# Kernel tuning notes

Measured on AMD Instinct MI355X. Metric: run time of the kernel, lower is better.

The kernel has to match this reference:

```python
import jax, jax.numpy as jnp
import numpy as np


def setup_inputs() -> dict:
    key = jax.random.key(0)
    ks = jax.random.split(key, 8)
    B, C, H, W = 8, 256, 64, 64
    Cqk = C // 8
    x = jax.random.normal(ks[0], (B, C, H, W), dtype=jnp.float32)
    # 1x1 conv weights, stored as [out_ch, in_ch] (kernel is 1x1)
    Wq = jax.random.normal(ks[1], (Cqk, C), dtype=jnp.float32) * 0.02
    bq = jnp.zeros((Cqk,), dtype=jnp.float32)
    Wk = jax.random.normal(ks[2], (Cqk, C), dtype=jnp.float32) * 0.02
    bk = jnp.zeros((Cqk,), dtype=jnp.float32)
    Wv = jax.random.normal(ks[3], (C, C), dtype=jnp.float32) * 0.02
    bv = jnp.zeros((C,), dtype=jnp.float32)
    # gamma initialized to zero in the module; use small nonzero so grads flow through attention path meaningfully
    gamma = jnp.asarray([0.5], dtype=jnp.float32)
    return {"x": x, "Wq": Wq, "bq": bq, "Wk": Wk, "bk": bk, "Wv": Wv, "bv": bv, "gamma": gamma}


def reference(x, Wq, bq, Wk, bk, Wv, bv, gamma):
    B, C, H, W = x.shape
    N = H * W
    xf = x.reshape(B, C, N)  # [B, C, N]
    # 1x1 convs == channel-wise matmuls
    q = jnp.einsum('oc,bcn->bno', Wq, xf) + bq  # [B, N, Cqk]
    k = jnp.einsum('oc,bcn->bon', Wk, xf) + bk[None, :, None]  # [B, Cqk, N]
    v = jnp.einsum('oc,bcn->bon', Wv, xf) + bv[None, :, None]  # [B, C, N]
    energy = jnp.einsum('bnd,bdm->bnm', q, k)  # [B, N, N], unscaled as in original
    attn = jax.nn.softmax(energy, axis=-1)
    out = jnp.einsum('bcm,bnm->bcn', v, attn)  # out[:, :, n] = sum_m v[:, :, m] * attn[n, m]
    out = out.reshape(B, C, H, W)
    return gamma[0] * out + x
```

## Files before the change

### kernel.cpp

```cpp
#include <hip/hip_runtime.h>
#include <hip/hip_bf16.h>

#define NB 8
#define CH 256
#define NN 4096
#define CQK 32
#define LOG2E 1.4426950408889634f

typedef __attribute__((ext_vector_type(4))) float f32x4;
typedef __attribute__((ext_vector_type(8))) short bf16x8;
typedef unsigned short u16;

static __device__ __forceinline__ u16 f2bf(float f) {
  unsigned int u = __float_as_uint(f);
  unsigned int r = (u + 0x7fffu + ((u >> 16) & 1u)) >> 16;
  return (u16)r;
}

__global__ void prep_weights(const float* __restrict__ Wq, const float* __restrict__ bq,
                             const float* __restrict__ Wk, const float* __restrict__ bk,
                             const float* __restrict__ Wv,
                             u16* __restrict__ Wqkf, u16* __restrict__ Wvf,
                             float* __restrict__ bqk) {
  int i = blockIdx.x * 256 + threadIdx.x;
  int o = i >> 8, c = i & 255;
  int kk = c >> 5, g2 = (c >> 3) & 3, j = c & 7;
  if (o < 64) {
    float wv = (o < 32) ? Wq[o * 256 + c] * LOG2E : Wk[(o - 32) * 256 + c];
    Wqkf[((((o >> 4) * 8 + kk) * 4 + g2) * 16 + (o & 15)) * 8 + j] = f2bf(wv);
  }
  Wvf[((((o >> 4) * 8 + kk) * 4 + g2) * 16 + (o & 15)) * 8 + j] = f2bf(Wv[i]);
  if (i < 64) bqk[i] = (i < 32) ? bq[i] * LOG2E : bk[i - 32];
}

__global__ __launch_bounds__(256, 2) void fused_proj(
    const float* __restrict__ x, const u16* __restrict__ Wqkf,
    const u16* __restrict__ Wvf, const float* __restrict__ bqk,
    const float* __restrict__ bv,
    u16* __restrict__ qbuf, u16* __restrict__ kbuf, u16* __restrict__ vbuf) {
  __shared__ __align__(128) char xt[64 * 512];
  const int b = blockIdx.y, n0 = blockIdx.x * 64;
  const int tid = threadIdx.x, w = tid >> 6, l = tid & 63, g = l >> 4, lr = l & 15;
  const f32x4 fzero = {0.f, 0.f, 0.f, 0.f};

  {
    const int nl = l, cl = w;
    const float* xp = x + (size_t)b * CH * NN + n0 + nl;
    char* xrow = xt + nl * 512;
    const int swz = (nl & 15) << 4;
#pragma unroll
    for (int p = 0; p < 32; ++p) {
      const int c = p * 8 + cl * 2;
      float f0 = xp[(size_t)c * NN], f1 = xp[(size_t)(c + 1) * NN];
      unsigned int pk = (unsigned int)f2bf(f0) | ((unsigned int)f2bf(f1) << 16);
      *(unsigned int*)(xrow + ((c * 2) ^ swz)) = pk;
    }
  }
  __syncthreads();

  const int aswz = lr << 4;

  {
    f32x4 acc[4];
#pragma unroll
    for (int ct = 0; ct < 4; ++ct) acc[ct] = fzero;
#pragma unroll
    for (int kk = 0; kk < 8; ++kk) {
      bf16x8 af = *(const bf16x8*)(xt + (w * 16 + lr) * 512 + ((kk * 64 + g * 16) ^ aswz));
#pragma unroll
      for (int ct = 0; ct < 4; ++ct) {
        bf16x8 bf = *(const bf16x8*)(Wqkf + (size_t)(((ct * 8 + kk) * 4 + g) * 16 + lr) * 8);
        acc[ct] = __builtin_amdgcn_mfma_f32_16x16x32_bf16(af, bf, acc[ct], 0, 0, 0);
      }
    }
#pragma unroll
    for (int ct = 0; ct < 4; ++ct) {
      const int col = ct * 16 + lr;
      const float bc = bqk[col];
#pragma unroll
      for (int r = 0; r < 4; ++r) {
        const int row = n0 + w * 16 + g * 4 + r;
        u16 h = f2bf(acc[ct][r] + bc);
        if (col < 32) qbuf[((size_t)(b * NN + row)) * 32 + col] = h;
        else          kbuf[((size_t)(b * NN + row)) * 32 + (col - 32)] = h;
      }
    }
  }

  {
    f32x4 vacc[4][4];
#pragma unroll
    for (int ct = 0; ct < 4; ++ct)
#pragma unroll
      for (int mt = 0; mt < 4; ++mt) vacc[ct][mt] = fzero;
#pragma unroll
    for (int kk = 0; kk < 8; ++kk) {
      bf16x8 bfm[4];
#pragma unroll
      for (int mt = 0; mt < 4; ++mt)
        bfm[mt] = *(const bf16x8*)(xt + (mt * 16 + lr) * 512 + ((kk * 64 + g * 16) ^ aswz));
#pragma unroll
      for (int ct = 0; ct < 4; ++ct) {
        bf16x8 af = *(const bf16x8*)(Wvf + (size_t)((((w * 4 + ct) * 8 + kk) * 4 + g) * 16 + lr) * 8);
#pragma unroll
        for (int mt = 0; mt < 4; ++mt)
          vacc[ct][mt] = __builtin_amdgcn_mfma_f32_16x16x32_bf16(af, bfm[mt], vacc[ct][mt], 0, 0, 0);
      }
    }
#pragma unroll
    for (int ct = 0; ct < 4; ++ct) {
#pragma unroll
      for (int mt = 0; mt < 4; ++mt) {
        const int m = n0 + mt * 16 + lr;
#pragma unroll
        for (int r = 0; r < 4; ++r) {
          const int ch = w * 64 + ct * 16 + g * 4 + r;
          vbuf[((size_t)(b * 128 + (m >> 5)) * 256 + ch) * 32 + (m & 31)] = f2bf(vacc[ct][mt][r] + bv[ch]);
        }
      }
    }
  }
}

#define KLOAD(t, sub) (*(const bf16x8*)(kp + (size_t)((((t) & 63) * 64) + (sub) * 16) * 32))
#define VLOAD(mg, ct) (*(const bf16x8*)(vp + (size_t)((mg) & 127) * 8192 + (ct) * 512))

#define EXPP(S, PW, MASK) {                                                                   \
  float e0 = __builtin_amdgcn_exp2f(S[0]);                                                    \
  float e1 = __builtin_amdgcn_exp2f(S[1]);                                                    \
  float e2 = __builtin_amdgcn_exp2f(S[2]);                                                    \
  float e3 = __builtin_amdgcn_exp2f(S[3]);                                                    \
  lsum += (MASK) * ((e0 + e1) + (e2 + e3));                                                   \
  PW.x = __builtin_amdgcn_perm(__float_as_uint(e1) + 0x8000u, __float_as_uint(e0) + 0x8000u, 0x07060302u); \
  PW.y = __builtin_amdgcn_perm(__float_as_uint(e3) + 0x8000u, __float_as_uint(e2) + 0x8000u, 0x07060302u); \
}

#define PBAR() do {                                  \
  __builtin_amdgcn_sched_barrier(0);                 \
  asm volatile("s_waitcnt lgkmcnt(0)");              \
  __builtin_amdgcn_s_barrier();                      \
  __builtin_amdgcn_sched_barrier(0);                 \
} while (0)

#define PVPH(BUF, NEXTMG) {                                                                   \
  const char* prb = (const char*)Pb + (BUF) * 16384;                                          \
  char* pdst = (char*)Pb + ((BUF) ^ 1) * 16384 + prow * 128;                                  \
  *(uint2*)(pdst + ((0 * 32 + g * 8) ^ wswz)) = pw0;                                          \
  *(uint2*)(pdst + ((1 * 32 + g * 8) ^ wswz)) = pw1;                                          \
  *(uint2*)(pdst + ((2 * 32 + g * 8) ^ wswz)) = pw2;                                          \
  *(uint2*)(pdst + ((3 * 32 + g * 8) ^ wswz)) = pw3;                                          \
  __builtin_amdgcn_s_setprio(1);                                                              \
  _Pragma("unroll")                                                                           \
  for (int nt = 0; nt < 4; ++nt) {                                                            \
    const int row = qg * 64 + nt * 16 + lr;                                                   \
    const int rs = (row & 7) << 4;                                                            \
    bf16x8 pa = *(const bf16x8*)(prb + row * 128 + ((g * 16) ^ rs));                          \
    oacc[nt][0] = __builtin_amdgcn_mfma_f32_16x16x32_bf16(vA0, pa, oacc[nt][0], 0, 0, 0);     \
    oacc[nt][1] = __builtin_amdgcn_mfma_f32_16x16x32_bf16(vA1, pa, oacc[nt][1], 0, 0, 0);     \
    oacc[nt][2] = __builtin_amdgcn_mfma_f32_16x16x32_bf16(vA2, pa, oacc[nt][2], 0, 0, 0);     \
    oacc[nt][3] = __builtin_amdgcn_mfma_f32_16x16x32_bf16(vA3, pa, oacc[nt][3], 0, 0, 0);     \
  }                                                                                           \
  vA0 = VLOAD(NEXTMG, 0); vA1 = VLOAD(NEXTMG, 1);                                             \
  vA2 = VLOAD(NEXTMG, 2); vA3 = VLOAD(NEXTMG, 3);                                             \
  _Pragma("unroll")                                                                           \
  for (int nt = 0; nt < 4; ++nt) {                                                            \
    const int row = qg * 64 + nt * 16 + lr;                                                   \
    const int rs = (row & 7) << 4;                                                            \
    bf16x8 pa = *(const bf16x8*)(prb + row * 128 + ((64 + g * 16) ^ rs));                     \
    oacc[nt][0] = __builtin_amdgcn_mfma_f32_16x16x32_bf16(vB0, pa, oacc[nt][0], 0, 0, 0);     \
    oacc[nt][1] = __builtin_amdgcn_mfma_f32_16x16x32_bf16(vB1, pa, oacc[nt][1], 0, 0, 0);     \
    oacc[nt][2] = __builtin_amdgcn_mfma_f32_16x16x32_bf16(vB2, pa, oacc[nt][2], 0, 0, 0);     \
    oacc[nt][3] = __builtin_amdgcn_mfma_f32_16x16x32_bf16(vB3, pa, oacc[nt][3], 0, 0, 0);     \
  }                                                                                           \
  __builtin_amdgcn_s_setprio(0);                                                              \
}

__global__ __launch_bounds__(512, 2) void attn_fused(
    const u16* __restrict__ qb, const u16* __restrict__ kbuf,
    const u16* __restrict__ vbuf, const float* __restrict__ x,
    const float* __restrict__ gamma_p, float* __restrict__ out) {
  __shared__ __align__(128) char Pb[2][128 * 128];
  __shared__ float lsum_s[128];

  const int b = blockIdx.x;
  const int n0 = blockIdx.y * 128;
  const int tid = threadIdx.x, w = tid >> 6, l = tid & 63, g = l >> 4, lr = l & 15;
  const int qg = w >> 2, cg = w & 3;
  const float gamma0 = gamma_p[0];
  const f32x4 fzero = {0.f, 0.f, 0.f, 0.f};

  bf16x8 qf = *(const bf16x8*)(qb + ((size_t)b * NN + n0 + w * 16 + lr) * 32 + g * 8);

  const u16* kp = kbuf + (size_t)b * (NN * 32) + (size_t)lr * 32 + g * 8;
  const u16* vp = vbuf + (size_t)b * 1048576 + (size_t)(cg * 64 + lr) * 32 + g * 8;

  f32x4 oacc[4][4];
#pragma unroll
  for (int nt = 0; nt < 4; ++nt)
#pragma unroll
    for (int ct = 0; ct < 4; ++ct) oacc[nt][ct] = fzero;
  float lsum = 0.f;

  const int prow = w * 16 + lr;
  const int wswz = (prow & 7) << 4;

  bf16x8 kA0 = KLOAD(0, 0), kA1 = KLOAD(0, 1), kA2 = KLOAD(0, 2), kA3 = KLOAD(0, 3);
  bf16x8 vA0 = VLOAD(0, 0), vA1 = VLOAD(0, 1), vA2 = VLOAD(0, 2), vA3 = VLOAD(0, 3);
  bf16x8 kB0 = KLOAD(1, 0), kB1 = KLOAD(1, 1), kB2 = KLOAD(1, 2), kB3 = KLOAD(1, 3);
  bf16x8 vB0, vB1, vB2, vB3;
  uint2 pw0, pw1, pw2, pw3;
  {
    f32x4 s0 = __builtin_amdgcn_mfma_f32_16x16x32_bf16(kA0, qf, fzero, 0, 0, 0);
    f32x4 s1 = __builtin_amdgcn_mfma_f32_16x16x32_bf16(kA1, qf, fzero, 0, 0, 0);
    f32x4 s2 = __builtin_amdgcn_mfma_f32_16x16x32_bf16(kA2, qf, fzero, 0, 0, 0);
    f32x4 s3 = __builtin_amdgcn_mfma_f32_16x16x32_bf16(kA3, qf, fzero, 0, 0, 0);
    EXPP(s0, pw0, 1.0f); EXPP(s1, pw1, 1.0f); EXPP(s2, pw2, 1.0f); EXPP(s3, pw3, 1.0f);
    char* pdst = (char*)Pb + prow * 128;
    *(uint2*)(pdst + ((0 * 32 + g * 8) ^ wswz)) = pw0;
    *(uint2*)(pdst + ((1 * 32 + g * 8) ^ wswz)) = pw1;
    *(uint2*)(pdst + ((2 * 32 + g * 8) ^ wswz)) = pw2;
    *(uint2*)(pdst + ((3 * 32 + g * 8) ^ wswz)) = pw3;
  }

  for (int it2 = 0; it2 < 32; ++it2) {
    {
      const int tn = 2 * it2 + 1;
      f32x4 s0 = __builtin_amdgcn_mfma_f32_16x16x32_bf16(kB0, qf, fzero, 0, 0, 0);
      f32x4 s1 = __builtin_amdgcn_mfma_f32_16x16x32_bf16(kB1, qf, fzero, 0, 0, 0);
      f32x4 s2 = __builtin_amdgcn_mfma_f32_16x16x32_bf16(kB2, qf, fzero, 0, 0, 0);
      f32x4 s3 = __builtin_amdgcn_mfma_f32_16x16x32_bf16(kB3, qf, fzero, 0, 0, 0);
      kA0 = KLOAD(tn + 1, 0); kA1 = KLOAD(tn + 1, 1); kA2 = KLOAD(tn + 1, 2); kA3 = KLOAD(tn + 1, 3);
      vB0 = VLOAD(4 * it2 + 1, 0); vB1 = VLOAD(4 * it2 + 1, 1);
      vB2 = VLOAD(4 * it2 + 1, 2); vB3 = VLOAD(4 * it2 + 1, 3);
      EXPP(s0, pw0, 1.0f); EXPP(s1, pw1, 1.0f); EXPP(s2, pw2, 1.0f); EXPP(s3, pw3, 1.0f);
      PBAR();
      PVPH(0, 4 * it2 + 2);
    }
    {
      const int tn = 2 * it2 + 2;
      const float tmask = (it2 < 31) ? 1.0f : 0.0f;
      f32x4 s0 = __builtin_amdgcn_mfma_f32_16x16x32_bf16(kA0, qf, fzero, 0, 0, 0);
      f32x4 s1 = __builtin_amdgcn_mfma_f32_16x16x32_bf16(kA1, qf, fzero, 0, 0, 0);
      f32x4 s2 = __builtin_amdgcn_mfma_f32_16x16x32_bf16(kA2, qf, fzero, 0, 0, 0);
      f32x4 s3 = __builtin_amdgcn_mfma_f32_16x16x32_bf16(kA3, qf, fzero, 0, 0, 0);
      kB0 = KLOAD(tn + 1, 0); kB1 = KLOAD(tn + 1, 1); kB2 = KLOAD(tn + 1, 2); kB3 = KLOAD(tn + 1, 3);
      vB0 = VLOAD(4 * it2 + 3, 0); vB1 = VLOAD(4 * it2 + 3, 1);
      vB2 = VLOAD(4 * it2 + 3, 2); vB3 = VLOAD(4 * it2 + 3, 3);
      EXPP(s0, pw0, tmask); EXPP(s1, pw1, tmask); EXPP(s2, pw2, tmask); EXPP(s3, pw3, tmask);
      PBAR();
      PVPH(1, 4 * it2 + 4);
    }
  }

  lsum += __shfl_xor(lsum, 16);
  lsum += __shfl_xor(lsum, 32);
  if (l < 16) lsum_s[w * 16 + lr] = lsum;
  __syncthreads();

  const size_t bbase = (size_t)b * CH * NN;
#pragma unroll
  for (int nt = 0; nt < 4; ++nt) {
    const int q = qg * 64 + nt * 16 + lr;
    const float linv = 1.f / lsum_s[q];
    const int n = n0 + q;
#pragma unroll
    for (int ct = 0; ct < 4; ++ct) {
      const int cbase = cg * 64 + ct * 16 + g * 4;
#pragma unroll
      for (int r = 0; r < 4; ++r) {
        const size_t off = bbase + (size_t)(cbase + r) * NN + n;
        out[off] = gamma0 * (oacc[nt][ct][r] * linv) + x[off];
      }
    }
  }
}

extern "C" void kernel_launch(void* const* d_in, const int* in_sizes, int n_in,
                              void* d_out, int out_size, void* d_ws, size_t ws_size,
                              hipStream_t stream) {
  const float* x     = (const float*)d_in[0];
  const float* Wq    = (const float*)d_in[1];
  const float* bq    = (const float*)d_in[2];
  const float* Wk    = (const float*)d_in[3];
  const float* bk    = (const float*)d_in[4];
  const float* Wv    = (const float*)d_in[5];
  const float* bv    = (const float*)d_in[6];
  const float* gamma = (const float*)d_in[7];
  float* out = (float*)d_out;

  char* ws = (char*)d_ws;
  u16*   qbuf = (u16*)(ws);
  u16*   kbuf = (u16*)(ws + 2097152);
  u16*   vbuf = (u16*)(ws + 4194304);
  u16*   Wqkf = (u16*)(ws + 20971520);
  u16*   Wvf  = (u16*)(ws + 21004288);
  float* bqk  = (float*)(ws + 21135360);

  prep_weights<<<256, 256, 0, stream>>>(Wq, bq, Wk, bk, Wv, Wqkf, Wvf, bqk);
  fused_proj<<<dim3(64, 8), 256, 0, stream>>>(x, Wqkf, Wvf, bqk, bv, qbuf, kbuf, vbuf);
  attn_fused<<<dim3(8, 32), 512, 0, stream>>>(qbuf, kbuf, vbuf, x, gamma, out);
}
```

Baseline: 127.0 us.

## Split attention output channels across two blocks with 4-wave blocks

The attention kernel now launches two blocks per query tile, each owning half of the output channels and running 4 waves instead of 8. Each wave computes scores for all 128 query rows (two Q fragments), writes both halves of P to shared memory, and accumulates 32 channels over 128 rows. This doubles the grid to 512 blocks, which may fill the CUs better, but the QK^T and exp work is now done twice, once per channel half.

```diff
diff --git a/kernel.cpp b/kernel.cpp
--- a/kernel.cpp
+++ b/kernel.cpp
@@ -125,12 +125,12 @@
 #define KLOAD(t, sub) (*(const bf16x8*)(kp + (size_t)((((t) & 63) * 64) + (sub) * 16) * 32))
 #define VLOAD(mg, ct) (*(const bf16x8*)(vp + (size_t)((mg) & 127) * 8192 + (ct) * 512))
 
-#define EXPP(S, PW, MASK) {                                                                   \
+#define EXPP(S, PW, MASK, LS) {                                                               \
   float e0 = __builtin_amdgcn_exp2f(S[0]);                                                    \
   float e1 = __builtin_amdgcn_exp2f(S[1]);                                                    \
   float e2 = __builtin_amdgcn_exp2f(S[2]);                                                    \
   float e3 = __builtin_amdgcn_exp2f(S[3]);                                                    \
-  lsum += (MASK) * ((e0 + e1) + (e2 + e3));                                                   \
+  LS += (MASK) * ((e0 + e1) + (e2 + e3));                                                     \
   PW.x = __builtin_amdgcn_perm(__float_as_uint(e1) + 0x8000u, __float_as_uint(e0) + 0x8000u, 0x07060302u); \
   PW.y = __builtin_amdgcn_perm(__float_as_uint(e3) + 0x8000u, __float_as_uint(e2) + 0x8000u, 0x07060302u); \
 }
@@ -142,40 +142,34 @@
   __builtin_amdgcn_sched_barrier(0);                 \
 } while (0)
 
-#define PVPH(BUF, NEXTMG) {                                                                   \
+#define PVPHASE(BUF, V0, V1, V2, V3) {                                                        \
   const char* prb = (const char*)Pb + (BUF) * 16384;                                          \
-  char* pdst = (char*)Pb + ((BUF) ^ 1) * 16384 + prow * 128;                                  \
+  char* pdst = (char*)Pb + ((BUF) ^ 1) * 16384 + prow0 * 128;                                 \
   *(uint2*)(pdst + ((0 * 32 + g * 8) ^ wswz)) = pw0;                                          \
   *(uint2*)(pdst + ((1 * 32 + g * 8) ^ wswz)) = pw1;                                          \
   *(uint2*)(pdst + ((2 * 32 + g * 8) ^ wswz)) = pw2;                                          \
   *(uint2*)(pdst + ((3 * 32 + g * 8) ^ wswz)) = pw3;                                          \
+  pdst += 64 * 128;                                                                           \
+  *(uint2*)(pdst + ((0 * 32 + g * 8) ^ wswz)) = pw4;                                          \
+  *(uint2*)(pdst + ((1 * 32 + g * 8) ^ wswz)) = pw5;                                          \
+  *(uint2*)(pdst + ((2 * 32 + g * 8) ^ wswz)) = pw6;                                          \
+  *(uint2*)(pdst + ((3 * 32 + g * 8) ^ wswz)) = pw7;                                          \
   __builtin_amdgcn_s_setprio(1);                                                              \
   _Pragma("unroll")                                                                           \
-  for (int nt = 0; nt < 4; ++nt) {                                                            \
-    const int row = qg * 64 + nt * 16 + lr;                                                   \
+  for (int nt = 0; nt < 8; ++nt) {                                                            \
+    const int row = nt * 16 + lr;                                                             \
     const int rs = (row & 7) << 4;                                                            \
-    bf16x8 pa = *(const bf16x8*)(prb + row * 128 + ((g * 16) ^ rs));                          \
-    oacc[nt][0] = __builtin_amdgcn_mfma_f32_16x16x32_bf16(vA0, pa, oacc[nt][0], 0, 0, 0);     \
-    oacc[nt][1] = __builtin_amdgcn_mfma_f32_16x16x32_bf16(vA1, pa, oacc[nt][1], 0, 0, 0);     \
-    oacc[nt][2] = __builtin_amdgcn_mfma_f32_16x16x32_bf16(vA2, pa, oacc[nt][2], 0, 0, 0);     \
-    oacc[nt][3] = __builtin_amdgcn_mfma_f32_16x16x32_bf16(vA3, pa, oacc[nt][3], 0, 0, 0);     \
-  }                                                                                           \
-  vA0 = VLOAD(NEXTMG, 0); vA1 = VLOAD(NEXTMG, 1);                                             \
-  vA2 = VLOAD(NEXTMG, 2); vA3 = VLOAD(NEXTMG, 3);                                             \
-  _Pragma("unroll")                                                                           \
-  for (int nt = 0; nt < 4; ++nt) {                                                            \
-    const int row = qg * 64 + nt * 16 + lr;                                                   \
-    const int rs = (row & 7) << 4;                                                            \
-    bf16x8 pa = *(const bf16x8*)(prb + row * 128 + ((64 + g * 16) ^ rs));                     \
-    oacc[nt][0] = __builtin_amdgcn_mfma_f32_16x16x32_bf16(vB0, pa, oacc[nt][0], 0, 0, 0);     \
-    oacc[nt][1] = __builtin_amdgcn_mfma_f32_16x16x32_bf16(vB1, pa, oacc[nt][1], 0, 0, 0);     \
-    oacc[nt][2] = __builtin_amdgcn_mfma_f32_16x16x32_bf16(vB2, pa, oacc[nt][2], 0, 0, 0);     \
-    oacc[nt][3] = __builtin_amdgcn_mfma_f32_16x16x32_bf16(vB3, pa, oacc[nt][3], 0, 0, 0);     \
+    bf16x8 pa0 = *(const bf16x8*)(prb + row * 128 + ((g * 16) ^ rs));                         \
+    bf16x8 pa1 = *(const bf16x8*)(prb + row * 128 + ((64 + g * 16) ^ rs));                    \
+    oacc[nt][0] = __builtin_amdgcn_mfma_f32_16x16x32_bf16(V0, pa0, oacc[nt][0], 0, 0, 0);     \
+    oacc[nt][1] = __builtin_amdgcn_mfma_f32_16x16x32_bf16(V1, pa0, oacc[nt][1], 0, 0, 0);     \
+    oacc[nt][0] = __builtin_amdgcn_mfma_f32_16x16x32_bf16(V2, pa1, oacc[nt][0], 0, 0, 0);     \
+    oacc[nt][1] = __builtin_amdgcn_mfma_f32_16x16x32_bf16(V3, pa1, oacc[nt][1], 0, 0, 0);     \
   }                                                                                           \
   __builtin_amdgcn_s_setprio(0);                                                              \
 }
 
-__global__ __launch_bounds__(512, 2) void attn_fused(
+__global__ __launch_bounds__(256, 2) void attn_fused(
     const u16* __restrict__ qb, const u16* __restrict__ kbuf,
     const u16* __restrict__ vbuf, const float* __restrict__ x,
     const float* __restrict__ gamma_p, float* __restrict__ out) {
@@ -184,88 +178,120 @@
 
   const int b = blockIdx.x;
   const int n0 = blockIdx.y * 128;
+  const int chh = blockIdx.z;
   const int tid = threadIdx.x, w = tid >> 6, l = tid & 63, g = l >> 4, lr = l & 15;
-  const int qg = w >> 2, cg = w & 3;
   const float gamma0 = gamma_p[0];
   const f32x4 fzero = {0.f, 0.f, 0.f, 0.f};
 
-  bf16x8 qf = *(const bf16x8*)(qb + ((size_t)b * NN + n0 + w * 16 + lr) * 32 + g * 8);
+  bf16x8 qf0 = *(const bf16x8*)(qb + ((size_t)b * NN + n0 + w * 16 + lr) * 32 + g * 8);
+  bf16x8 qf1 = *(const bf16x8*)(qb + ((size_t)b * NN + n0 + 64 + w * 16 + lr) * 32 + g * 8);
 
   const u16* kp = kbuf + (size_t)b * (NN * 32) + (size_t)lr * 32 + g * 8;
-  const u16* vp = vbuf + (size_t)b * 1048576 + (size_t)(cg * 64 + lr) * 32 + g * 8;
-
-  f32x4 oacc[4][4];
-#pragma unroll
-  for (int nt = 0; nt < 4; ++nt)
-#pragma unroll
-    for (int ct = 0; ct < 4; ++ct) oacc[nt][ct] = fzero;
-  float lsum = 0.f;
-
-  const int prow = w * 16 + lr;
-  const int wswz = (prow & 7) << 4;
+  const u16* vp = vbuf + (size_t)b * 1048576 + (size_t)(chh * 128 + w * 32 + lr) * 32 + g * 8;
+
+  f32x4 oacc[8][2];
+#pragma unroll
+  for (int nt = 0; nt < 8; ++nt)
+#pragma unroll
+    for (int ct = 0; ct < 2; ++ct) oacc[nt][ct] = fzero;
+  float lsum0 = 0.f, lsum1 = 0.f;
+
+  const int prow0 = w * 16 + lr;
+  const int wswz = (prow0 & 7) << 4;
 
   bf16x8 kA0 = KLOAD(0, 0), kA1 = KLOAD(0, 1), kA2 = KLOAD(0, 2), kA3 = KLOAD(0, 3);
-  bf16x8 vA0 = VLOAD(0, 0), vA1 = VLOAD(0, 1), vA2 = VLOAD(0, 2), vA3 = VLOAD(0, 3);
+  bf16x8 vA0 = VLOAD(0, 0), vA1 = VLOAD(0, 1), vA2 = VLOAD(1, 0), vA3 = VLOAD(1, 1);
   bf16x8 kB0 = KLOAD(1, 0), kB1 = KLOAD(1, 1), kB2 = KLOAD(1, 2), kB3 = KLOAD(1, 3);
   bf16x8 vB0, vB1, vB2, vB3;
-  uint2 pw0, pw1, pw2, pw3;
+  uint2 pw0, pw1, pw2, pw3, pw4, pw5, pw6, pw7;
   {
-    f32x4 s0 = __builtin_amdgcn_mfma_f32_16x16x32_bf16(kA0, qf, fzero, 0, 0, 0);
-    f32x4 s1 = __builtin_amdgcn_mfma_f32_16x16x32_bf16(kA1, qf, fzero, 0, 0, 0);
-    f32x4 s2 = __builtin_amdgcn_mfma_f32_16x16x32_bf16(kA2, qf, fzero, 0, 0, 0);
-    f32x4 s3 = __builtin_amdgcn_mfma_f32_16x16x32_bf16(kA3, qf, fzero, 0, 0, 0);
-    EXPP(s0, pw0, 1.0f); EXPP(s1, pw1, 1.0f); EXPP(s2, pw2, 1.0f); EXPP(s3, pw3, 1.0f);
-    char* pdst = (char*)Pb + prow * 128;
+    f32x4 s0 = __builtin_amdgcn_mfma_f32_16x16x32_bf16(kA0, qf0, fzero, 0, 0, 0);
+    f32x4 s1 = __builtin_amdgcn_mfma_f32_16x16x32_bf16(kA1, qf0, fzero, 0, 0, 0);
+    f32x4 s2 = __builtin_amdgcn_mfma_f32_16x16x32_bf16(kA2, qf0, fzero, 0, 0, 0);
+    f32x4 s3 = __builtin_amdgcn_mfma_f32_16x16x32_bf16(kA3, qf0, fzero, 0, 0, 0);
+    f32x4 s4 = __builtin_amdgcn_mfma_f32_16x16x32_bf16(kA0, qf1, fzero, 0, 0, 0);
+    f32x4 s5 = __builtin_amdgcn_mfma_f32_16x16x32_bf16(kA1, qf1, fzero, 0, 0, 0);
+    f32x4 s6 = __builtin_amdgcn_mfma_f32_16x16x32_bf16(kA2, qf1, fzero, 0, 0, 0);
+    f32x4 s7 = __builtin_amdgcn_mfma_f32_16x16x32_bf16(kA3, qf1, fzero, 0, 0, 0);
+    EXPP(s0, pw0, 1.0f, lsum0); EXPP(s1, pw1, 1.0f, lsum0);
+    EXPP(s2, pw2, 1.0f, lsum0); EXPP(s3, pw3, 1.0f, lsum0);
+    EXPP(s4, pw4, 1.0f, lsum1); EXPP(s5, pw5, 1.0f, lsum1);
+    EXPP(s6, pw6, 1.0f, lsum1); EXPP(s7, pw7, 1.0f, lsum1);
+    char* pdst = (char*)Pb + prow0 * 128;
     *(uint2*)(pdst + ((0 * 32 + g * 8) ^ wswz)) = pw0;
     *(uint2*)(pdst + ((1 * 32 + g * 8) ^ wswz)) = pw1;
     *(uint2*)(pdst + ((2 * 32 + g * 8) ^ wswz)) = pw2;
     *(uint2*)(pdst + ((3 * 32 + g * 8) ^ wswz)) = pw3;
+    pdst += 64 * 128;
+    *(uint2*)(pdst + ((0 * 32 + g * 8) ^ wswz)) = pw4;
+    *(uint2*)(pdst + ((1 * 32 + g * 8) ^ wswz)) = pw5;
+    *(uint2*)(pdst + ((2 * 32 + g * 8) ^ wswz)) = pw6;
+    *(uint2*)(pdst + ((3 * 32 + g * 8) ^ wswz)) = pw7;
   }
 
   for (int it2 = 0; it2 < 32; ++it2) {
     {
       const int tn = 2 * it2 + 1;
-      f32x4 s0 = __builtin_amdgcn_mfma_f32_16x16x32_bf16(kB0, qf, fzero, 0, 0, 0);
-      f32x4 s1 = __builtin_amdgcn_mfma_f32_16x16x32_bf16(kB1, qf, fzero, 0, 0, 0);
-      f32x4 s2 = __builtin_amdgcn_mfma_f32_16x16x32_bf16(kB2, qf, fzero, 0, 0, 0);
-      f32x4 s3 = __builtin_amdgcn_mfma_f32_16x16x32_bf16(kB3, qf, fzero, 0, 0, 0);
+      f32x4 s0 = __builtin_amdgcn_mfma_f32_16x16x32_bf16(kB0, qf0, fzero, 0, 0, 0);
+      f32x4 s1 = __builtin_amdgcn_mfma_f32_16x16x32_bf16(kB1, qf0, fzero, 0, 0, 0);
+      f32x4 s2 = __builtin_amdgcn_mfma_f32_16x16x32_bf16(kB2, qf0, fzero, 0, 0, 0);
+      f32x4 s3 = __builtin_amdgcn_mfma_f32_16x16x32_bf16(kB3, qf0, fzero, 0, 0, 0);
+      f32x4 s4 = __builtin_amdgcn_mfma_f32_16x16x32_bf16(kB0, qf1, fzero, 0, 0, 0);
+      f32x4 s5 = __builtin_amdgcn_mfma_f32_16x16x32_bf16(kB1, qf1, fzero, 0, 0, 0);
+      f32x4 s6 = __builtin_amdgcn_mfma_f32_16x16x32_bf16(kB2, qf1, fzero, 0, 0, 0);
+      f32x4 s7 = __builtin_amdgcn_mfma_f32_16x16x32_bf16(kB3, qf1, fzero, 0, 0, 0);
       kA0 = KLOAD(tn + 1, 0); kA1 = KLOAD(tn + 1, 1); kA2 = KLOAD(tn + 1, 2); kA3 = KLOAD(tn + 1, 3);
-      vB0 = VLOAD(4 * it2 + 1, 0); vB1 = VLOAD(4 * it2 + 1, 1);
-      vB2 = VLOAD(4 * it2 + 1, 2); vB3 = VLOAD(4 * it2 + 1, 3);
-      EXPP(s0, pw0, 1.0f); EXPP(s1, pw1, 1.0f); EXPP(s2, pw2, 1.0f); EXPP(s3, pw3, 1.0f);
+      vB0 = VLOAD(2 * tn, 0); vB1 = VLOAD(2 * tn, 1);
+      vB2 = VLOAD(2 * tn + 1, 0); vB3 = VLOAD(2 * tn + 1, 1);
+      EXPP(s0, pw0, 1.0f, lsum0); EXPP(s1, pw1, 1.0f, lsum0);
+      EXPP(s2, pw2, 1.0f, lsum0); EXPP(s3, pw3, 1.0f, lsum0);
+      EXPP(s4, pw4, 1.0f, lsum1); EXPP(s5, pw5, 1.0f, lsum1);
+      EXPP(s6, pw6, 1.0f, lsum1); EXPP(s7, pw7, 1.0f, lsum1);
       PBAR();
-      PVPH(0, 4 * it2 + 2);
+      PVPHASE(0, vA0, vA1, vA2, vA3);
     }
     {
       const int tn = 2 * it2 + 2;
       const float tmask = (it2 < 31) ? 1.0f : 0.0f;
-      f32x4 s0 = __builtin_amdgcn_mfma_f32_16x16x32_bf16(kA0, qf, fzero, 0, 0, 0);
-      f32x4 s1 = __builtin_amdgcn_mfma_f32_16x16x32_bf16(kA1, qf, fzero, 0, 0, 0);
-      f32x4 s2 = __builtin_amdgcn_mfma_f32_16x16x32_bf16(kA2, qf, fzero, 0, 0, 0);
-      f32x4 s3 = __builtin_amdgcn_mfma_f32_16x16x32_bf16(kA3, qf, fzero, 0, 0, 0);
+      f32x4 s0 = __builtin_amdgcn_mfma_f32_16x16x32_bf16(kA0, qf0, fzero, 0, 0, 0);
+      f32x4 s1 = __builtin_amdgcn_mfma_f32_16x16x32_bf16(kA1, qf0, fzero, 0, 0, 0);
+      f32x4 s2 = __builtin_amdgcn_mfma_f32_16x16x32_bf16(kA2, qf0, fzero, 0, 0, 0);
+      f32x4 s3 = __builtin_amdgcn_mfma_f32_16x16x32_bf16(kA3, qf0, fzero, 0, 0, 0);
+      f32x4 s4 = __builtin_amdgcn_mfma_f32_16x16x32_bf16(kA0, qf1, fzero, 0, 0, 0);
+      f32x4 s5 = __builtin_amdgcn_mfma_f32_16x16x32_bf16(kA1, qf1, fzero, 0, 0, 0);
+      f32x4 s6 = __builtin_amdgcn_mfma_f32_16x16x32_bf16(kA2, qf1, fzero, 0, 0, 0);
+      f32x4 s7 = __builtin_amdgcn_mfma_f32_16x16x32_bf16(kA3, qf1, fzero, 0, 0, 0);
       kB0 = KLOAD(tn + 1, 0); kB1 = KLOAD(tn + 1, 1); kB2 = KLOAD(tn + 1, 2); kB3 = KLOAD(tn + 1, 3);
-      vB0 = VLOAD(4 * it2 + 3, 0); vB1 = VLOAD(4 * it2 + 3, 1);
-      vB2 = VLOAD(4 * it2 + 3, 2); vB3 = VLOAD(4 * it2 + 3, 3);
-      EXPP(s0, pw0, tmask); EXPP(s1, pw1, tmask); EXPP(s2, pw2, tmask); EXPP(s3, pw3, tmask);
+      vA0 = VLOAD(2 * tn, 0); vA1 = VLOAD(2 * tn, 1);
+      vA2 = VLOAD(2 * tn + 1, 0); vA3 = VLOAD(2 * tn + 1, 1);
+      EXPP(s0, pw0, tmask, lsum0); EXPP(s1, pw1, tmask, lsum0);
+      EXPP(s2, pw2, tmask, lsum0); EXPP(s3, pw3, tmask, lsum0);
+      EXPP(s4, pw4, tmask, lsum1); EXPP(s5, pw5, tmask, lsum1);
+      EXPP(s6, pw6, tmask, lsum1); EXPP(s7, pw7, tmask, lsum1);
       PBAR();
-      PVPH(1, 4 * it2 + 4);
-    }
-  }
-
-  lsum += __shfl_xor(lsum, 16);
-  lsum += __shfl_xor(lsum, 32);
-  if (l < 16) lsum_s[w * 16 + lr] = lsum;
+      PVPHASE(1, vB0, vB1, vB2, vB3);
+    }
+  }
+
+  lsum0 += __shfl_xor(lsum0, 16);
+  lsum0 += __shfl_xor(lsum0, 32);
+  lsum1 += __shfl_xor(lsum1, 16);
+  lsum1 += __shfl_xor(lsum1, 32);
+  if (l < 16) {
+    lsum_s[w * 16 + lr] = lsum0;
+    lsum_s[64 + w * 16 + lr] = lsum1;
+  }
   __syncthreads();
 
   const size_t bbase = (size_t)b * CH * NN;
 #pragma unroll
-  for (int nt = 0; nt < 4; ++nt) {
-    const int q = qg * 64 + nt * 16 + lr;
+  for (int nt = 0; nt < 8; ++nt) {
+    const int q = nt * 16 + lr;
     const float linv = 1.f / lsum_s[q];
     const int n = n0 + q;
 #pragma unroll
-    for (int ct = 0; ct < 4; ++ct) {
-      const int cbase = cg * 64 + ct * 16 + g * 4;
+    for (int ct = 0; ct < 2; ++ct) {
+      const int cbase = chh * 128 + w * 32 + ct * 16 + g * 4;
 #pragma unroll
       for (int r = 0; r < 4; ++r) {
         const size_t off = bbase + (size_t)(cbase + r) * NN + n;
@@ -298,5 +324,5 @@
 
   prep_weights<<<256, 256, 0, stream>>>(Wq, bq, Wk, bk, Wv, Wqkf, Wvf, bqk);
   fused_proj<<<dim3(64, 8), 256, 0, stream>>>(x, Wqkf, Wvf, bqk, bv, qbuf, kbuf, vbuf);
-  attn_fused<<<dim3(8, 32), 512, 0, stream>>>(qbuf, kbuf, vbuf, x, gamma, out);
-}
+  attn_fused<<<dim3(8, 32, 2), 256, 0, stream>>>(qbuf, kbuf, vbuf, x, gamma, out);
+}
```

Result: no change. 125.3 us (-1.4%).

## Widen key tile to 128 per step and split PV work by channel only

Applied to the files above, without the earlier changes.

Each iteration now processes 128 keys instead of 64, so there are 16 double-iterations instead of 32 and half as many block barriers. The P tile in LDS doubles to 128x128 per buffer. The PV stage is repartitioned so each wave owns 32 output channels across all 128 query rows, instead of 64 channels by 64 rows. That cuts redundant P reads per V fragment and changes V load reuse. The cost is more registers for K fragments and a larger LDS footprint, which may lower occupancy.

```diff
diff --git a/kernel.cpp b/kernel.cpp
--- a/kernel.cpp
+++ b/kernel.cpp
@@ -122,7 +122,7 @@
   }
 }
 
-#define KLOAD(t, sub) (*(const bf16x8*)(kp + (size_t)((((t) & 63) * 64) + (sub) * 16) * 32))
+#define KLOAD2(T, sub) (*(const bf16x8*)(kp + (size_t)((((T) & 31) * 128) + (sub) * 16) * 32))
 #define VLOAD(mg, ct) (*(const bf16x8*)(vp + (size_t)((mg) & 127) * 8192 + (ct) * 512))
 
 #define EXPP(S, PW, MASK) {                                                                   \
@@ -142,113 +142,118 @@
   __builtin_amdgcn_sched_barrier(0);                 \
 } while (0)
 
-#define PVPH(BUF, NEXTMG) {                                                                   \
-  const char* prb = (const char*)Pb + (BUF) * 16384;                                          \
-  char* pdst = (char*)Pb + ((BUF) ^ 1) * 16384 + prow * 128;                                  \
+#define QK8(K0, K1, K2, K3, K4, K5, K6, K7, MASK) {                                           \
+  f32x4 s0 = __builtin_amdgcn_mfma_f32_16x16x32_bf16(K0, qf, fzero, 0, 0, 0);                 \
+  f32x4 s1 = __builtin_amdgcn_mfma_f32_16x16x32_bf16(K1, qf, fzero, 0, 0, 0);                 \
+  f32x4 s2 = __builtin_amdgcn_mfma_f32_16x16x32_bf16(K2, qf, fzero, 0, 0, 0);                 \
+  f32x4 s3 = __builtin_amdgcn_mfma_f32_16x16x32_bf16(K3, qf, fzero, 0, 0, 0);                 \
+  f32x4 s4 = __builtin_amdgcn_mfma_f32_16x16x32_bf16(K4, qf, fzero, 0, 0, 0);                 \
+  f32x4 s5 = __builtin_amdgcn_mfma_f32_16x16x32_bf16(K5, qf, fzero, 0, 0, 0);                 \
+  f32x4 s6 = __builtin_amdgcn_mfma_f32_16x16x32_bf16(K6, qf, fzero, 0, 0, 0);                 \
+  f32x4 s7 = __builtin_amdgcn_mfma_f32_16x16x32_bf16(K7, qf, fzero, 0, 0, 0);                 \
+  EXPP(s0, pw0, MASK); EXPP(s1, pw1, MASK); EXPP(s2, pw2, MASK); EXPP(s3, pw3, MASK);         \
+  EXPP(s4, pw4, MASK); EXPP(s5, pw5, MASK); EXPP(s6, pw6, MASK); EXPP(s7, pw7, MASK);         \
+}
+
+#define PWRITE(BUF) {                                                                         \
+  char* pdst = (char*)Pb + (BUF) * 32768 + prow * 256;                                        \
   *(uint2*)(pdst + ((0 * 32 + g * 8) ^ wswz)) = pw0;                                          \
   *(uint2*)(pdst + ((1 * 32 + g * 8) ^ wswz)) = pw1;                                          \
   *(uint2*)(pdst + ((2 * 32 + g * 8) ^ wswz)) = pw2;                                          \
   *(uint2*)(pdst + ((3 * 32 + g * 8) ^ wswz)) = pw3;                                          \
-  __builtin_amdgcn_s_setprio(1);                                                              \
+  *(uint2*)(pdst + ((4 * 32 + g * 8) ^ wswz)) = pw4;                                          \
+  *(uint2*)(pdst + ((5 * 32 + g * 8) ^ wswz)) = pw5;                                          \
+  *(uint2*)(pdst + ((6 * 32 + g * 8) ^ wswz)) = pw6;                                          \
+  *(uint2*)(pdst + ((7 * 32 + g * 8) ^ wswz)) = pw7;                                          \
+}
+
+#define PVQ(PRB, QTR, VA, VB) {                                                               \
   _Pragma("unroll")                                                                           \
-  for (int nt = 0; nt < 4; ++nt) {                                                            \
-    const int row = qg * 64 + nt * 16 + lr;                                                   \
+  for (int nt = 0; nt < 8; ++nt) {                                                            \
+    const int row = nt * 16 + lr;                                                             \
     const int rs = (row & 7) << 4;                                                            \
-    bf16x8 pa = *(const bf16x8*)(prb + row * 128 + ((g * 16) ^ rs));                          \
-    oacc[nt][0] = __builtin_amdgcn_mfma_f32_16x16x32_bf16(vA0, pa, oacc[nt][0], 0, 0, 0);     \
-    oacc[nt][1] = __builtin_amdgcn_mfma_f32_16x16x32_bf16(vA1, pa, oacc[nt][1], 0, 0, 0);     \
-    oacc[nt][2] = __builtin_amdgcn_mfma_f32_16x16x32_bf16(vA2, pa, oacc[nt][2], 0, 0, 0);     \
-    oacc[nt][3] = __builtin_amdgcn_mfma_f32_16x16x32_bf16(vA3, pa, oacc[nt][3], 0, 0, 0);     \
+    bf16x8 pa = *(const bf16x8*)((PRB) + row * 256 + (((QTR) * 64 + g * 16) ^ rs));           \
+    oacc[nt][0] = __builtin_amdgcn_mfma_f32_16x16x32_bf16(VA, pa, oacc[nt][0], 0, 0, 0);      \
+    oacc[nt][1] = __builtin_amdgcn_mfma_f32_16x16x32_bf16(VB, pa, oacc[nt][1], 0, 0, 0);      \
   }                                                                                           \
-  vA0 = VLOAD(NEXTMG, 0); vA1 = VLOAD(NEXTMG, 1);                                             \
-  vA2 = VLOAD(NEXTMG, 2); vA3 = VLOAD(NEXTMG, 3);                                             \
-  _Pragma("unroll")                                                                           \
-  for (int nt = 0; nt < 4; ++nt) {                                                            \
-    const int row = qg * 64 + nt * 16 + lr;                                                   \
-    const int rs = (row & 7) << 4;                                                            \
-    bf16x8 pa = *(const bf16x8*)(prb + row * 128 + ((64 + g * 16) ^ rs));                     \
-    oacc[nt][0] = __builtin_amdgcn_mfma_f32_16x16x32_bf16(vB0, pa, oacc[nt][0], 0, 0, 0);     \
-    oacc[nt][1] = __builtin_amdgcn_mfma_f32_16x16x32_bf16(vB1, pa, oacc[nt][1], 0, 0, 0);     \
-    oacc[nt][2] = __builtin_amdgcn_mfma_f32_16x16x32_bf16(vB2, pa, oacc[nt][2], 0, 0, 0);     \
-    oacc[nt][3] = __builtin_amdgcn_mfma_f32_16x16x32_bf16(vB3, pa, oacc[nt][3], 0, 0, 0);     \
-  }                                                                                           \
-  __builtin_amdgcn_s_setprio(0);                                                              \
 }
 
 __global__ __launch_bounds__(512, 2) void attn_fused(
     const u16* __restrict__ qb, const u16* __restrict__ kbuf,
     const u16* __restrict__ vbuf, const float* __restrict__ x,
     const float* __restrict__ gamma_p, float* __restrict__ out) {
-  __shared__ __align__(128) char Pb[2][128 * 128];
+  __shared__ __align__(128) char Pb[2][128 * 256];
   __shared__ float lsum_s[128];
 
   const int b = blockIdx.x;
   const int n0 = blockIdx.y * 128;
   const int tid = threadIdx.x, w = tid >> 6, l = tid & 63, g = l >> 4, lr = l & 15;
-  const int qg = w >> 2, cg = w & 3;
   const float gamma0 = gamma_p[0];
   const f32x4 fzero = {0.f, 0.f, 0.f, 0.f};
 
   bf16x8 qf = *(const bf16x8*)(qb + ((size_t)b * NN + n0 + w * 16 + lr) * 32 + g * 8);
 
   const u16* kp = kbuf + (size_t)b * (NN * 32) + (size_t)lr * 32 + g * 8;
-  const u16* vp = vbuf + (size_t)b * 1048576 + (size_t)(cg * 64 + lr) * 32 + g * 8;
-
-  f32x4 oacc[4][4];
-#pragma unroll
-  for (int nt = 0; nt < 4; ++nt)
-#pragma unroll
-    for (int ct = 0; ct < 4; ++ct) oacc[nt][ct] = fzero;
+  const u16* vp = vbuf + (size_t)b * 1048576 + (size_t)(w * 32 + lr) * 32 + g * 8;
+
+  f32x4 oacc[8][2];
+#pragma unroll
+  for (int nt = 0; nt < 8; ++nt)
+#pragma unroll
+    for (int ct = 0; ct < 2; ++ct) oacc[nt][ct] = fzero;
   float lsum = 0.f;
 
   const int prow = w * 16 + lr;
   const int wswz = (prow & 7) << 4;
 
-  bf16x8 kA0 = KLOAD(0, 0), kA1 = KLOAD(0, 1), kA2 = KLOAD(0, 2), kA3 = KLOAD(0, 3);
-  bf16x8 vA0 = VLOAD(0, 0), vA1 = VLOAD(0, 1), vA2 = VLOAD(0, 2), vA3 = VLOAD(0, 3);
-  bf16x8 kB0 = KLOAD(1, 0), kB1 = KLOAD(1, 1), kB2 = KLOAD(1, 2), kB3 = KLOAD(1, 3);
-  bf16x8 vB0, vB1, vB2, vB3;
-  uint2 pw0, pw1, pw2, pw3;
-  {
-    f32x4 s0 = __builtin_amdgcn_mfma_f32_16x16x32_bf16(kA0, qf, fzero, 0, 0, 0);
-    f32x4 s1 = __builtin_amdgcn_mfma_f32_16x16x32_bf16(kA1, qf, fzero, 0, 0, 0);
-    f32x4 s2 = __builtin_amdgcn_mfma_f32_16x16x32_bf16(kA2, qf, fzero, 0, 0, 0);
-    f32x4 s3 = __builtin_amdgcn_mfma_f32_16x16x32_bf16(kA3, qf, fzero, 0, 0, 0);
-    EXPP(s0, pw0, 1.0f); EXPP(s1, pw1, 1.0f); EXPP(s2, pw2, 1.0f); EXPP(s3, pw3, 1.0f);
-    char* pdst = (char*)Pb + prow * 128;
-    *(uint2*)(pdst + ((0 * 32 + g * 8) ^ wswz)) = pw0;
-    *(uint2*)(pdst + ((1 * 32 + g * 8) ^ wswz)) = pw1;
-    *(uint2*)(pdst + ((2 * 32 + g * 8) ^ wswz)) = pw2;
-    *(uint2*)(pdst + ((3 * 32 + g * 8) ^ wswz)) = pw3;
-  }
-
-  for (int it2 = 0; it2 < 32; ++it2) {
+  bf16x8 kA0 = KLOAD2(0, 0), kA1 = KLOAD2(0, 1), kA2 = KLOAD2(0, 2), kA3 = KLOAD2(0, 3);
+  bf16x8 kA4 = KLOAD2(0, 4), kA5 = KLOAD2(0, 5), kA6 = KLOAD2(0, 6), kA7 = KLOAD2(0, 7);
+  bf16x8 kB0 = KLOAD2(1, 0), kB1 = KLOAD2(1, 1), kB2 = KLOAD2(1, 2), kB3 = KLOAD2(1, 3);
+  bf16x8 kB4 = KLOAD2(1, 4), kB5 = KLOAD2(1, 5), kB6 = KLOAD2(1, 6), kB7 = KLOAD2(1, 7);
+  bf16x8 v0, v1, v2, v3, v4, v5, v6, v7;
+  uint2 pw0, pw1, pw2, pw3, pw4, pw5, pw6, pw7;
+  QK8(kA0, kA1, kA2, kA3, kA4, kA5, kA6, kA7, 1.0f);
+  PWRITE(0);
+
+  for (int T2 = 0; T2 < 16; ++T2) {
     {
-      const int tn = 2 * it2 + 1;
-      f32x4 s0 = __builtin_amdgcn_mfma_f32_16x16x32_bf16(kB0, qf, fzero, 0, 0, 0);
-      f32x4 s1 = __builtin_amdgcn_mfma_f32_16x16x32_bf16(kB1, qf, fzero, 0, 0, 0);
-      f32x4 s2 = __builtin_amdgcn_mfma_f32_16x16x32_bf16(kB2, qf, fzero, 0, 0, 0);
-      f32x4 s3 = __builtin_amdgcn_mfma_f32_16x16x32_bf16(kB3, qf, fzero, 0, 0, 0);
-      kA0 = KLOAD(tn + 1, 0); kA1 = KLOAD(tn + 1, 1); kA2 = KLOAD(tn + 1, 2); kA3 = KLOAD(tn + 1, 3);
-      vB0 = VLOAD(4 * it2 + 1, 0); vB1 = VLOAD(4 * it2 + 1, 1);
-      vB2 = VLOAD(4 * it2 + 1, 2); vB3 = VLOAD(4 * it2 + 1, 3);
-      EXPP(s0, pw0, 1.0f); EXPP(s1, pw1, 1.0f); EXPP(s2, pw2, 1.0f); EXPP(s3, pw3, 1.0f);
+      const int T = 2 * T2;
+      v0 = VLOAD(4 * T, 0); v1 = VLOAD(4 * T, 1);
+      v2 = VLOAD(4 * T + 1, 0); v3 = VLOAD(4 * T + 1, 1);
+      QK8(kB0, kB1, kB2, kB3, kB4, kB5, kB6, kB7, 1.0f);
+      kA0 = KLOAD2(T + 2, 0); kA1 = KLOAD2(T + 2, 1); kA2 = KLOAD2(T + 2, 2); kA3 = KLOAD2(T + 2, 3);
+      kA4 = KLOAD2(T + 2, 4); kA5 = KLOAD2(T + 2, 5); kA6 = KLOAD2(T + 2, 6); kA7 = KLOAD2(T + 2, 7);
       PBAR();
-      PVPH(0, 4 * it2 + 2);
+      PWRITE(1);
+      v4 = VLOAD(4 * T + 2, 0); v5 = VLOAD(4 * T + 2, 1);
+      v6 = VLOAD(4 * T + 3, 0); v7 = VLOAD(4 * T + 3, 1);
+      const char* prb = (const char*)Pb;
+      __builtin_amdgcn_s_setprio(1);
+      PVQ(prb, 0, v0, v1);
+      PVQ(prb, 1, v2, v3);
+      PVQ(prb, 2, v4, v5);
+      PVQ(prb, 3, v6, v7);
+      __builtin_amdgcn_s_setprio(0);
     }
     {
-      const int tn = 2 * it2 + 2;
-      const float tmask = (it2 < 31) ? 1.0f : 0.0f;
-      f32x4 s0 = __builtin_amdgcn_mfma_f32_16x16x32_bf16(kA0, qf, fzero, 0, 0, 0);
-      f32x4 s1 = __builtin_amdgcn_mfma_f32_16x16x32_bf16(kA1, qf, fzero, 0, 0, 0);
-      f32x4 s2 = __builtin_amdgcn_mfma_f32_16x16x32_bf16(kA2, qf, fzero, 0, 0, 0);
-      f32x4 s3 = __builtin_amdgcn_mfma_f32_16x16x32_bf16(kA3, qf, fzero, 0, 0, 0);
-      kB0 = KLOAD(tn + 1, 0); kB1 = KLOAD(tn + 1, 1); kB2 = KLOAD(tn + 1, 2); kB3 = KLOAD(tn + 1, 3);
-      vB0 = VLOAD(4 * it2 + 3, 0); vB1 = VLOAD(4 * it2 + 3, 1);
-      vB2 = VLOAD(4 * it2 + 3, 2); vB3 = VLOAD(4 * it2 + 3, 3);
-      EXPP(s0, pw0, tmask); EXPP(s1, pw1, tmask); EXPP(s2, pw2, tmask); EXPP(s3, pw3, tmask);
+      const int T = 2 * T2 + 1;
+      const float tmask = (T2 < 15) ? 1.0f : 0.0f;
+      v0 = VLOAD(4 * T, 0); v1 = VLOAD(4 * T, 1);
+      v2 = VLOAD(4 * T + 1, 0); v3 = VLOAD(4 * T + 1, 1);
+      QK8(kA0, kA1, kA2, kA3, kA4, kA5, kA6, kA7, tmask);
+      kB0 = KLOAD2(T + 2, 0); kB1 = KLOAD2(T + 2, 1); kB2 = KLOAD2(T + 2, 2); kB3 = KLOAD2(T + 2, 3);
+      kB4 = KLOAD2(T + 2, 4); kB5 = KLOAD2(T + 2, 5); kB6 = KLOAD2(T + 2, 6); kB7 = KLOAD2(T + 2, 7);
       PBAR();
-      PVPH(1, 4 * it2 + 4);
+      PWRITE(0);
+      v4 = VLOAD(4 * T + 2, 0); v5 = VLOAD(4 * T + 2, 1);
+      v6 = VLOAD(4 * T + 3, 0); v7 = VLOAD(4 * T + 3, 1);
+      const char* prb = (const char*)Pb + 32768;
+      __builtin_amdgcn_s_setprio(1);
+      PVQ(prb, 0, v0, v1);
+      PVQ(prb, 1, v2, v3);
+      PVQ(prb, 2, v4, v5);
+      PVQ(prb, 3, v6, v7);
+      __builtin_amdgcn_s_setprio(0);
     }
   }
 
@@ -259,13 +264,13 @@
 
   const size_t bbase = (size_t)b * CH * NN;
 #pragma unroll
-  for (int nt = 0; nt < 4; ++nt) {
-    const int q = qg * 64 + nt * 16 + lr;
+  for (int nt = 0; nt < 8; ++nt) {
+    const int q = nt * 16 + lr;
     const float linv = 1.f / lsum_s[q];
     const int n = n0 + q;
 #pragma unroll
-    for (int ct = 0; ct < 4; ++ct) {
-      const int cbase = cg * 64 + ct * 16 + g * 4;
+    for (int ct = 0; ct < 2; ++ct) {
+      const int cbase = w * 32 + ct * 16 + g * 4;
 #pragma unroll
       for (int r = 0; r < 4; ++r) {
         const size_t off = bbase + (size_t)(cbase + r) * NN + n;
```

Result: faster. 112.6 us (-11.3%).
